# Kernel tuning notes

Hardware: AMD Instinct MI355X
Metric: run time of the kernel (lower is better)

The kernel has to match this reference:

```python
import jax, jax.numpy as jnp
import numpy as np

L_LAYERS = 4
B = 8
PATCH_H = 37
PATCH_W = 37
P = PATCH_H * PATCH_W  # 1369
D = 1024
J = 768
H = 518
W = 518
R_LIST = [1, 3, 5]
K_LIST = [1, 2, 3]
TOPMIN_MIN = 0.0
TOPMIN_MAX = 0.3


def setup_inputs() -> dict:
    key = jax.random.key(0)
    k1, k2 = jax.random.split(key)
    features = jax.random.normal(k1, (L_LAYERS, B, P, D), dtype=jnp.float32)
    cls_tokens = jax.random.normal(k2, (B, J), dtype=jnp.float32)
    return {"features": features, "cls_tokens": cls_tokens}


def _layer_norm_2d(x, eps=1e-5):
    # torch.layer_norm with normalized_shape = (P, D): normalize jointly over last two dims, no affine
    mu = jnp.mean(x, axis=(-2, -1), keepdims=True)
    var = jnp.var(x, axis=(-2, -1), keepdims=True)
    return (x - mu) * jax.lax.rsqrt(var + eps)


def _lnamd(features, r):
    # LNAMD: unfold(r,r, zero pad r//2) + adaptive_avg_pool1d(D*r*r -> D) == per-channel r x r
    # neighborhood mean over the patch grid with zero padding (pool bins are exactly r*r wide).
    if r == 1:
        return features
    l, b, p, d = features.shape
    x = features.reshape(l * b, PATCH_H, PATCH_W, d)
    pad = r // 2
    s = jax.lax.reduce_window(x, 0.0, jax.lax.add, (1, r, r, 1), (1, 1, 1, 1),
                              [(0, 0), (pad, pad), (pad, pad), (0, 0)])
    return (s / float(r * r)).reshape(l, b, p, d)


def _msm(rf, use_remat=False):
    # rf: [L,B,P,D] L2-normalized. Mutual scoring: for each image i, euclidean cdist of its
    # patches to all other images' patches, min over ref patches, mean of [k_min:k_max] smallest.
    l, b, p, d = rf.shape
    k_min = int(TOPMIN_MIN * (b - 1))
    k_max = int(TOPMIN_MAX * (b - 1))
    sq = jnp.sum(rf * rf, axis=-1)  # [L,B,P]

    def per_image(i):
        feat = rf[:, i]  # [L,P,D]
        dots = jnp.einsum('lpd,lbqd->lpbq', feat, rf)  # [L,P,B,P]
        d2 = sq[:, i][:, :, None, None] + sq[:, None, :, :] - 2.0 * dots
        dist = jnp.sqrt(jnp.maximum(d2, 1e-12))
        mind = jnp.min(dist, axis=-1)  # [L,P,B]
        mind = jnp.where(jnp.arange(b)[None, None, :] == i, jnp.inf, mind)  # exclude self
        neg_top = jax.lax.top_k(-mind, k_max)[0]  # k_max smallest distances (ascending)
        sel = -neg_top[..., k_min:k_max]
        return jnp.mean(sel, axis=-1)  # [L,P]

    fn = jax.checkpoint(per_image) if use_remat else per_image
    scores = jax.lax.map(fn, jnp.arange(b))  # [B,L,P]; lax.map keeps one cdist block live at a time
    return jnp.transpose(scores, (1, 0, 2))  # [L,B,P]


def _rscin(sim, scores, top_k):
    # zero out the B-top_k smallest similarities per row (keep top_k largest), row-normalize, reweight
    b = sim.shape[0]
    if top_k < b:
        vals, idx = jax.lax.top_k(sim, top_k)
        masked = jnp.zeros_like(sim).at[jnp.arange(b)[:, None], idx].set(vals)
    else:
        masked = sim
    masked = masked / jnp.sum(masked, axis=-1, keepdims=True)
    return masked @ scores


def _interp_mat(out_len, in_len):
    # bilinear, align_corners=True: src = dst * (in-1)/(out-1); separable 1D interpolation matrix
    pos = jnp.arange(out_len, dtype=jnp.float32) * ((in_len - 1) / (out_len - 1))
    i0 = jnp.clip(jnp.floor(pos).astype(jnp.int32), 0, in_len - 1)
    i1 = jnp.minimum(i0 + 1, in_len - 1)
    w = pos - i0.astype(jnp.float32)
    m = jnp.zeros((out_len, in_len), jnp.float32)
    m = m.at[jnp.arange(out_len), i0].add(1.0 - w)
    m = m.at[jnp.arange(out_len), i1].add(w)
    return m


def _forward(features, cls_tokens, use_remat=False):
    feats = _layer_norm_2d(features)  # [L,B,P,D]
    per_r = []
    for r in R_LIST:
        rf = _lnamd(feats, r)
        rf = rf / jnp.linalg.norm(rf, axis=-1, keepdims=True)
        per_r.append(jnp.mean(_msm(rf, use_remat), axis=0))  # mean over layers -> [B,P]
    scores = jnp.mean(jnp.stack(per_r, axis=0), axis=0)  # [B,P]
    img_scores = jnp.max(scores, axis=1)  # [B]
    cls = cls_tokens / jnp.linalg.norm(cls_tokens, axis=-1, keepdims=True)
    sim = cls @ cls.T  # [B,B]
    final = jnp.mean(jnp.stack([_rscin(sim, img_scores, k) for k in K_LIST], axis=0), axis=0)
    patch = scores.reshape(-1, PATCH_H, PATCH_W)
    mh = _interp_mat(H, PATCH_H)
    mw = _interp_mat(W, PATCH_W)
    pixel = jnp.einsum('Hh,bhw,Ww->bHW', mh, patch, mw)  # [B,H,W]
    return final, pixel


def reference(features, cls_tokens):
    return _forward(features, cls_tokens)
```

## Files before the change

### kernel.cpp

```cpp
#include <hip/hip_runtime.h>
#include <hip/hip_bf16.h>
#include <math.h>

#define L_LAYERS 4
#define BIMG 8
#define PATCH_H 37
#define PATCH_W 37
#define PP 1369
#define DD 1024
#define JJ 768
#define HOUT 518
#define WOUT 518
#define PPAD 1408
#define NPAIR 28
#define ZPAIR (L_LAYERS * NPAIR)
#define RFSZ  ((size_t)L_LAYERS * BIMG * PPAD * DD)
#define NRMSZ ((size_t)L_LAYERS * BIMG * PPAD)
#define MINDSZ ((size_t)L_LAYERS * BIMG * BIMG * PP)

typedef float floatx4 __attribute__((ext_vector_type(4)));

__device__ __forceinline__ unsigned int f2e4m3(float v) {
  unsigned int b = __float_as_uint(v);
  unsigned int sign = (b >> 24) & 0x80u;
  float mag = fabsf(v);
  unsigned int code;
  if (mag >= 0.015625f) {
    unsigned int mb = __float_as_uint(mag);
    mb = mb + 0x0007ffffu + ((mb >> 20) & 1u);
    code = (((mb >> 23) - 120u) << 3) | ((mb >> 20) & 7u);
  } else {
    code = (unsigned int)__float2int_rn(mag * 512.0f);
  }
  return code | sign;
}
__device__ __forceinline__ float e4m3tof(unsigned int c) {
  unsigned int em = c & 0x7fu;
  float m;
  if (em >= 8u) m = __uint_as_float((((em >> 3) + 120u) << 23) | ((em & 7u) << 20));
  else          m = (float)em * 0.001953125f;
  return (c & 0x80u) ? -m : m;
}

__device__ __forceinline__ int rf_swz(int p, int d) {
  return (d & ~63) |
         ((((d >> 4) & 3) ^ ((p >> 2) & 3)) << 4) |
         ((((d >> 3) & 1) ^ ((p >> 1) & 1)) << 3) |
         (d & 7);
}

__device__ __forceinline__ void gload_lds16(const void* gptr, void* lptr) {
  __builtin_amdgcn_global_load_lds(
      (const __attribute__((address_space(1))) unsigned int*)gptr,
      (__attribute__((address_space(3))) unsigned int*)lptr, 16, 0, 0);
}

__global__ __launch_bounds__(256) void k1_mu(const float* __restrict__ x,
                                             float* __restrict__ mu_acc) {
  const int lb = blockIdx.y;
  const float* base = x + (size_t)lb * PP * DD;
  const int N4 = PP * DD / 4;
  float s = 0.0f;
  for (int idx = blockIdx.x * 256 + threadIdx.x; idx < N4; idx += gridDim.x * 256) {
    float4 u = *(const float4*)(base + (size_t)idx * 4);
    s += u.x + u.y + u.z + u.w;
  }
  for (int off = 1; off < 64; off <<= 1) s += __shfl_xor(s, off, 64);
  __shared__ float red[4];
  if ((threadIdx.x & 63) == 0) red[threadIdx.x >> 6] = s;
  __syncthreads();
  if (threadIdx.x == 0)
    atomicAdd(&mu_acc[lb], red[0] + red[1] + red[2] + red[3]);
}

__device__ __forceinline__ void finish_r(float s0, float s1, float s2, float s3,
                                         float cm, unsigned char* dst, float* nrmdst,
                                         int tid, float* red) {
  s0 -= cm; s1 -= cm; s2 -= cm; s3 -= cm;
  float sq = s0 * s0 + s1 * s1 + s2 * s2 + s3 * s3;
  for (int off = 1; off < 64; off <<= 1) sq += __shfl_xor(sq, off, 64);
  __syncthreads();
  if ((tid & 63) == 0) red[tid >> 6] = sq;
  __syncthreads();
  const float rn16 = rsqrtf(red[0] + red[1] + red[2] + red[3]) * 16.0f;
  unsigned int c0 = f2e4m3(s0 * rn16), c1 = f2e4m3(s1 * rn16);
  unsigned int c2 = f2e4m3(s2 * rn16), c3 = f2e4m3(s3 * rn16);
  uchar4 o; o.x = (unsigned char)c0; o.y = (unsigned char)c1;
  o.z = (unsigned char)c2; o.w = (unsigned char)c3;
  *(uchar4*)dst = o;
  float q0 = e4m3tof(c0), q1 = e4m3tof(c1), q2 = e4m3tof(c2), q3 = e4m3tof(c3);
  float nq = q0 * q0 + q1 * q1 + q2 * q2 + q3 * q3;
  for (int off = 1; off < 64; off <<= 1) nq += __shfl_xor(nq, off, 64);
  __syncthreads();
  if ((tid & 63) == 0) red[tid >> 6] = nq;
  __syncthreads();
  if (tid == 0) *nrmdst = red[0] + red[1] + red[2] + red[3];
}

__global__ __launch_bounds__(256) void k2_pool3(const float* __restrict__ x,
                                                const float* __restrict__ mu_acc,
                                                unsigned char* __restrict__ rf,
                                                float* __restrict__ nrm) {
  const int p  = blockIdx.x;
  const int lb = blockIdx.y;
  const int tid = threadIdx.x;
  const int d0 = tid * 4;
  if (p >= PP) {
    const size_t zoff = ((size_t)lb * PPAD + p) * DD + d0;
    uchar4 z; z.x = 0; z.y = 0; z.z = 0; z.w = 0;
    for (int r = 0; r < 3; r++) {
      *(uchar4*)(rf + r * RFSZ + zoff) = z;
      if (tid == 0) nrm[r * NRMSZ + (size_t)lb * PPAD + p] = 0.0f;
    }
    return;
  }
  const size_t outoff = ((size_t)lb * PPAD + p) * DD + rf_swz(p, d0);
  const float mu = mu_acc[lb] * (1.0f / ((float)PP * (float)DD));
  const int ph = p / PATCH_W, pw = p % PATCH_W;
  float a5[4] = {0, 0, 0, 0}, a3[4] = {0, 0, 0, 0}, a1[4] = {0, 0, 0, 0};
  int c5 = 0, c3 = 0;
  for (int dy = -2; dy <= 2; dy++) {
    int qh = ph + dy; if (qh < 0 || qh >= PATCH_H) continue;
    for (int dx = -2; dx <= 2; dx++) {
      int qw = pw + dx; if (qw < 0 || qw >= PATCH_W) continue;
      const float* src = x + ((size_t)lb * PP + qh * PATCH_W + qw) * DD + d0;
      float4 u = *(const float4*)src;
      a5[0] += u.x; a5[1] += u.y; a5[2] += u.z; a5[3] += u.w; c5++;
      if (dy >= -1 && dy <= 1 && dx >= -1 && dx <= 1) {
        a3[0] += u.x; a3[1] += u.y; a3[2] += u.z; a3[3] += u.w; c3++;
        if (dy == 0 && dx == 0) { a1[0] = u.x; a1[1] = u.y; a1[2] = u.z; a1[3] = u.w; }
      }
    }
  }
  __shared__ float red[4];
  const size_t noff = (size_t)lb * PPAD + p;
  finish_r(a1[0], a1[1], a1[2], a1[3], mu, rf + outoff, nrm + noff, tid, red);
  finish_r(a3[0], a3[1], a3[2], a3[3], (float)c3 * mu, rf + RFSZ + outoff,
           nrm + NRMSZ + noff, tid, red);
  finish_r(a5[0], a5[1], a5[2], a5[3], (float)c5 * mu, rf + 2 * RFSZ + outoff,
           nrm + 2 * NRMSZ + noff, tid, red);
}

__global__ __launch_bounds__(256) void k2_pool(const float* __restrict__ x,
                                               const float* __restrict__ mu_acc,
                                               unsigned char* __restrict__ rf,
                                               float* __restrict__ nrm, int r) {
  const int p  = blockIdx.x;
  const int lb = blockIdx.y;
  const int tid = threadIdx.x;
  const int d0 = tid * 4;
  if (p >= PP) {
    const size_t zoff = ((size_t)lb * PPAD + p) * DD + d0;
    uchar4 z; z.x = 0; z.y = 0; z.z = 0; z.w = 0;
    *(uchar4*)(rf + zoff) = z;
    if (tid == 0) nrm[(size_t)lb * PPAD + p] = 0.0f;
    return;
  }
  const size_t outoff = ((size_t)lb * PPAD + p) * DD + rf_swz(p, d0);
  const float mu = mu_acc[lb] * (1.0f / ((float)PP * (float)DD));
  const int ph = p / PATCH_W, pw = p % PATCH_W;
  const int pad = r >> 1;
  float s0 = 0, s1 = 0, s2 = 0, s3 = 0;
  int cnt = 0;
  for (int dy = -pad; dy <= pad; dy++) {
    int qh = ph + dy; if (qh < 0 || qh >= PATCH_H) continue;
    for (int dx = -pad; dx <= pad; dx++) {
      int qw = pw + dx; if (qw < 0 || qw >= PATCH_W) continue;
      cnt++;
      const float* src = x + ((size_t)lb * PP + qh * PATCH_W + qw) * DD + d0;
      float4 u = *(const float4*)src;
      s0 += u.x; s1 += u.y; s2 += u.z; s3 += u.w;
    }
  }
  __shared__ float red[4];
  finish_r(s0, s1, s2, s3, (float)cnt * mu, rf + outoff,
           nrm + (size_t)lb * PPAD + p, tid, red);
}

__global__ __launch_bounds__(256, 4) void k3_pairdots(const unsigned char* __restrict__ rf,
                                                      const float* __restrict__ nrm,
                                                      unsigned int* __restrict__ mind) {
  const int rsel = blockIdx.z / ZPAIR;
  const int zz   = blockIdx.z % ZPAIR;
  const int l = zz / NPAIR;
  int rem = zz % NPAIR;
  int i = 0, span = BIMG - 1;
  while (rem >= span) { rem -= span; span--; i++; }
  const int j = i + 1 + rem;

  const unsigned char* rfr = rf + (size_t)rsel * RFSZ;
  const int rowbase = blockIdx.x * 128;
  const int colbase = blockIdx.y * 128;
  const unsigned char* A  = rfr + ((size_t)(l * BIMG + i) * PPAD + rowbase) * DD;
  const unsigned char* Bp = rfr + ((size_t)(l * BIMG + j) * PPAD + colbase) * DD;

  __shared__ __align__(16) unsigned char lA[2][128 * 64];
  __shared__ __align__(16) unsigned char lB[2][128 * 64];

  const int tid  = threadIdx.x;
  const int lane = tid & 63;
  const int wave = tid >> 6;
  const int lrow = lane & 15;
  const int quad = lane >> 4;
  const int wr = (wave >> 1) * 64;
  const int wc = (wave & 1) * 64;

  floatx4 acc[4][4];
#pragma unroll
  for (int a = 0; a < 4; a++)
#pragma unroll
    for (int b = 0; b < 4; b++) acc[a][b] = (floatx4){0.f, 0.f, 0.f, 0.f};

  const int r0  = wave * 32 + (lane >> 2);
  const size_t goff = (size_t)r0 * DD + (lane & 3) * 16;
  const int woff = wave * 2048;

  const int gs   = (lrow >> 2) & 3;
  const int hb   = (lrow >> 1) & 1;
  const int sub8 = (((quad & 1) ^ hb) << 3);

  gload_lds16(A + goff, lA[0] + woff);
  gload_lds16(A + goff + 16 * DD, lA[0] + woff + 1024);
  gload_lds16(Bp + goff, lB[0] + woff);
  gload_lds16(Bp + goff + 16 * DD, lB[0] + woff + 1024);
  __syncthreads();

#pragma unroll 2
  for (int t = 0; t < 16; ++t) {
    const int cur = t & 1;
    if (t < 15) {
      const int k1 = (t + 1) << 6;
      gload_lds16(A + goff + k1, lA[cur ^ 1] + woff);
      gload_lds16(A + goff + 16 * DD + k1, lA[cur ^ 1] + woff + 1024);
      gload_lds16(Bp + goff + k1, lB[cur ^ 1] + woff);
      gload_lds16(Bp + goff + 16 * DD + k1, lB[cur ^ 1] + woff + 1024);
    }
#pragma unroll
    for (int ks = 0; ks < 2; ks++) {
      const int gfrag = ((((ks << 1) + (quad >> 1)) ^ gs) << 4) + sub8;
      long af[4], bfv[4];
#pragma unroll
      for (int mt = 0; mt < 4; mt++)
        af[mt] = *(const long*)(lA[cur] + (wr + mt * 16 + lrow) * 64 + gfrag);
#pragma unroll
      for (int ct = 0; ct < 4; ct++)
        bfv[ct] = *(const long*)(lB[cur] + (wc + ct * 16 + lrow) * 64 + gfrag);
#pragma unroll
      for (int mt = 0; mt < 4; mt++)
#pragma unroll
        for (int ct = 0; ct < 4; ct++)
          acc[mt][ct] = __builtin_amdgcn_mfma_f32_16x16x32_fp8_fp8(
              af[mt], bfv[ct], acc[mt][ct], 0, 0, 0);
    }
    __syncthreads();
  }

  const float* nI = nrm + rsel * NRMSZ + (size_t)(l * BIMG + i) * PPAD;
  const float* nJ = nrm + rsel * NRMSZ + (size_t)(l * BIMG + j) * PPAD;
  unsigned int* mrow = mind + rsel * MINDSZ + ((size_t)(l * BIMG + i) * BIMG + j) * PP;
  unsigned int* mcol = mind + rsel * MINDSZ + ((size_t)(l * BIMG + j) * BIMG + i) * PP;

#pragma unroll
  for (int mt = 0; mt < 4; mt++) {
#pragma unroll
    for (int reg = 0; reg < 4; reg++) {
      const int gr = rowbase + wr + mt * 16 + quad * 4 + reg;
      float v = -1e30f;
#pragma unroll
      for (int ct = 0; ct < 4; ct++) {
        const int gc = colbase + wc + ct * 16 + lrow;
        if (gc < PP) v = fmaxf(v, 2.0f * acc[mt][ct][reg] - nJ[gc]);
      }
      for (int off = 1; off < 16; off <<= 1) v = fmaxf(v, __shfl_xor(v, off, 64));
      if (lrow == 0 && gr < PP)
        atomicMax(mrow + gr, __float_as_uint(v + 1024.0f));
    }
  }
#pragma unroll
  for (int ct = 0; ct < 4; ct++) {
    const int gc = colbase + wc + ct * 16 + lrow;
    float v = -1e30f;
#pragma unroll
    for (int mt = 0; mt < 4; mt++) {
      const int grb = rowbase + wr + mt * 16 + quad * 4;
#pragma unroll
      for (int reg = 0; reg < 4; reg++)
        if (grb + reg < PP) v = fmaxf(v, 2.0f * acc[mt][ct][reg] - nI[grb + reg]);
    }
    for (int off = 16; off < 64; off <<= 1) v = fmaxf(v, __shfl_xor(v, off, 64));
    if (quad == 0 && gc < PP)
      atomicMax(mcol + gc, __float_as_uint(v + 1024.0f));
  }
}

__global__ void k4_scores(const unsigned int* __restrict__ mind,
                          const float* __restrict__ nrm,
                          float* __restrict__ scores, int nr) {
  const int idx = blockIdx.x * 256 + threadIdx.x;
  if (idx >= BIMG * PP) return;
  const int i = idx / PP, p = idx % PP;
  float accum = 0.0f;
  for (int r = 0; r < nr; r++) {
    for (int l = 0; l < L_LAYERS; l++) {
      const float n_own = nrm[r * NRMSZ + (size_t)(l * BIMG + i) * PPAD + p];
      float m1 = 1e30f, m2 = 1e30f;
      for (int b = 0; b < BIMG; b++) {
        if (b == i) continue;
        const unsigned int enc =
            mind[r * MINDSZ + ((size_t)(l * BIMG + i) * BIMG + b) * PP + p];
        const float val = __uint_as_float(enc) - 1024.0f;
        const float d2 = fmaxf((n_own - val) * (1.0f / 256.0f), 1e-12f);
        const float dist = sqrtf(d2);
        if (dist < m1) { m2 = m1; m1 = dist; }
        else if (dist < m2) { m2 = dist; }
      }
      accum += 0.5f * (m1 + m2);
    }
  }
  scores[idx] += accum * (1.0f / (float)(L_LAYERS * 3));
}

__global__ void k5_imgmax(const float* __restrict__ scores, float* __restrict__ img) {
  const int i = blockIdx.x;
  float m = -1e30f;
  for (int p = threadIdx.x; p < PP; p += 256) m = fmaxf(m, scores[i * PP + p]);
  for (int off = 1; off < 64; off <<= 1) m = fmaxf(m, __shfl_xor(m, off, 64));
  __shared__ float red[4];
  if ((threadIdx.x & 63) == 0) red[threadIdx.x >> 6] = m;
  __syncthreads();
  if (threadIdx.x == 0)
    img[i] = fmaxf(fmaxf(red[0], red[1]), fmaxf(red[2], red[3]));
}

__global__ void k6_final(const float* __restrict__ cls,
                         const float* __restrict__ img,
                         float* __restrict__ out) {
  __shared__ float norms[BIMG];
  __shared__ float sim[BIMG][BIMG];
  const int t = threadIdx.x;
  if (t < BIMG) {
    float s = 0;
    for (int d = 0; d < JJ; d++) { float v = cls[t * JJ + d]; s += v * v; }
    norms[t] = sqrtf(s);
  }
  __syncthreads();
  {
    const int ii = t >> 3, jj = t & 7;
    float s = 0;
    for (int d = 0; d < JJ; d++) s += cls[ii * JJ + d] * cls[jj * JJ + d];
    sim[ii][jj] = s / (norms[ii] * norms[jj]);
  }
  __syncthreads();
  if (t < BIMG) {
    float v[8]; int id[8];
    for (int a = 0; a < 8; a++) { v[a] = sim[t][a]; id[a] = a; }
    for (int a = 0; a < 8; a++) {
      int best = a;
      for (int b = a + 1; b < 8; b++) if (v[b] > v[best]) best = b;
      float tv = v[a]; v[a] = v[best]; v[best] = tv;
      int ti = id[a]; id[a] = id[best]; id[best] = ti;
    }
    float res = 0;
    for (int k = 1; k <= 3; k++) {
      float num = 0, den = 0;
      for (int a = 0; a < k; a++) { num += v[a] * img[id[a]]; den += v[a]; }
      res += num / den;
    }
    out[t] = res * (1.0f / 3.0f);
  }
}

__global__ void k7_pixel(const float* __restrict__ scores,
                         float* __restrict__ out) {
  const int idx = blockIdx.x * 256 + threadIdx.x;
  if (idx >= BIMG * HOUT * WOUT) return;
  const int b = idx / (HOUT * WOUT);
  const int rem = idx % (HOUT * WOUT);
  const int Y = rem / WOUT, X = rem % WOUT;
  const float sy = (float)(PATCH_H - 1) / (float)(HOUT - 1);
  const float sx = (float)(PATCH_W - 1) / (float)(WOUT - 1);
  float py = (float)Y * sy;
  float px = (float)X * sx;
  int y0 = (int)floorf(py); y0 = min(max(y0, 0), PATCH_H - 1);
  int x0 = (int)floorf(px); x0 = min(max(x0, 0), PATCH_W - 1);
  const int y1 = min(y0 + 1, PATCH_H - 1);
  const int x1 = min(x0 + 1, PATCH_W - 1);
  const float wy = py - (float)y0, wx = px - (float)x0;
  const float* sc = scores + (size_t)b * PP;
  const float v =
      (1.f - wy) * ((1.f - wx) * sc[y0 * PATCH_W + x0] + wx * sc[y0 * PATCH_W + x1]) +
      wy         * ((1.f - wx) * sc[y1 * PATCH_W + x0] + wx * sc[y1 * PATCH_W + x1]);
  out[8 + idx] = v;
}

extern "C" void kernel_launch(void* const* d_in, const int* in_sizes, int n_in,
                              void* d_out, int out_size, void* d_ws, size_t ws_size,
                              hipStream_t stream) {
  const float* feat = (const float*)d_in[0];
  const float* cls  = (const float*)d_in[1];
  float* out = (float*)d_out;

  const size_t need_fused = 3 * RFSZ + 3 * MINDSZ * 4 + 3 * NRMSZ * 4 +
                            (size_t)BIMG * PP * 4 + 1024;
  const bool fused = ws_size >= need_fused;

  char* ws = (char*)d_ws;
  size_t off = 0;
  unsigned char* rf = (unsigned char*)(ws + off);
  off += (fused ? 3 : 1) * RFSZ;
  unsigned int* mind = (unsigned int*)(ws + off);
  off += (fused ? 3 : 1) * MINDSZ * 4;
  float* nrm = (float*)(ws + off);
  off += (fused ? 3 : 1) * NRMSZ * 4;
  float* scores = (float*)(ws + off);
  off += (size_t)BIMG * PP * 4;
  float* mu_acc = (float*)(ws + off);
  off += 32 * 4;
  float* img = (float*)(ws + off);
  off += 8 * 4;

  hipMemsetAsync(mu_acc, 0, 32 * 4, stream);
  hipMemsetAsync(scores, 0, (size_t)BIMG * PP * 4, stream);
  k1_mu<<<dim3(43, 32), 256, 0, stream>>>(feat, mu_acc);

  if (fused) {
    k2_pool3<<<dim3(PPAD, 32), 256, 0, stream>>>(feat, mu_acc, rf, nrm);
    hipMemsetAsync(mind, 0, 3 * MINDSZ * 4, stream);
    k3_pairdots<<<dim3(11, 11, 3 * ZPAIR), 256, 0, stream>>>(rf, nrm, mind);
    k4_scores<<<(BIMG * PP + 255) / 256, 256, 0, stream>>>(mind, nrm, scores, 3);
  } else {
    const int rlist[3] = {1, 3, 5};
    for (int ri = 0; ri < 3; ri++) {
      k2_pool<<<dim3(PPAD, 32), 256, 0, stream>>>(feat, mu_acc, rf, nrm, rlist[ri]);
      hipMemsetAsync(mind, 0, MINDSZ * 4, stream);
      k3_pairdots<<<dim3(11, 11, ZPAIR), 256, 0, stream>>>(rf, nrm, mind);
      k4_scores<<<(BIMG * PP + 255) / 256, 256, 0, stream>>>(mind, nrm, scores, 1);
    }
  }
  k5_imgmax<<<8, 256, 0, stream>>>(scores, img);
  k6_final<<<1, 64, 0, stream>>>(cls, img, out);
  k7_pixel<<<(BIMG * HOUT * WOUT + 255) / 256, 256, 0, stream>>>(scores, out);
}
```

Measured before the change: 2.571 ms.

## Remap pairdots grid for XCD locality and use fine-grained waitcnt pipelining

Flattens the pairdots launch to a 1D grid and remaps block IDs so that consecutive work tiles land on the same XCD (blockIdx mod 8 interleave). This is meant to improve L2 reuse of shared A/B panels. It also restructures the K loop: issue the next prefetch, wait only on the older loads with vmcnt(4), and use raw s_barrier with sched_barrier, with the last iteration peeled out. This replaces full __syncthreads and lets loads overlap compute, at the cost of depending on hand-coded waitcnt correctness. The remap assumes the grid size divides evenly by 8.

```diff
diff --git a/kernel.cpp b/kernel.cpp
--- a/kernel.cpp
+++ b/kernel.cpp
@@ -180,8 +180,15 @@
 __global__ __launch_bounds__(256, 4) void k3_pairdots(const unsigned char* __restrict__ rf,
                                                       const float* __restrict__ nrm,
                                                       unsigned int* __restrict__ mind) {
-  const int rsel = blockIdx.z / ZPAIR;
-  const int zz   = blockIdx.z % ZPAIR;
+  const unsigned int cpx = gridDim.x >> 3;
+  const unsigned int wid = (blockIdx.x & 7) * cpx + (blockIdx.x >> 3);
+  const int z  = wid / 121;
+  const int rm = wid % 121;
+  const int ty = rm / 11;
+  const int tx = rm % 11;
+
+  const int rsel = z / ZPAIR;
+  const int zz   = z % ZPAIR;
   const int l = zz / NPAIR;
   int rem = zz % NPAIR;
   int i = 0, span = BIMG - 1;
@@ -189,8 +196,8 @@
   const int j = i + 1 + rem;
 
   const unsigned char* rfr = rf + (size_t)rsel * RFSZ;
-  const int rowbase = blockIdx.x * 128;
-  const int colbase = blockIdx.y * 128;
+  const int rowbase = tx * 128;
+  const int colbase = ty * 128;
   const unsigned char* A  = rfr + ((size_t)(l * BIMG + i) * PPAD + rowbase) * DD;
   const unsigned char* Bp = rfr + ((size_t)(l * BIMG + j) * PPAD + colbase) * DD;
 
@@ -223,18 +230,17 @@
   gload_lds16(A + goff + 16 * DD, lA[0] + woff + 1024);
   gload_lds16(Bp + goff, lB[0] + woff);
   gload_lds16(Bp + goff + 16 * DD, lB[0] + woff + 1024);
-  __syncthreads();
-
-#pragma unroll 2
-  for (int t = 0; t < 16; ++t) {
+
+  for (int t = 0; t < 15; ++t) {
     const int cur = t & 1;
-    if (t < 15) {
-      const int k1 = (t + 1) << 6;
-      gload_lds16(A + goff + k1, lA[cur ^ 1] + woff);
-      gload_lds16(A + goff + 16 * DD + k1, lA[cur ^ 1] + woff + 1024);
-      gload_lds16(Bp + goff + k1, lB[cur ^ 1] + woff);
-      gload_lds16(Bp + goff + 16 * DD + k1, lB[cur ^ 1] + woff + 1024);
-    }
+    const int k1 = (t + 1) << 6;
+    gload_lds16(A + goff + k1, lA[cur ^ 1] + woff);
+    gload_lds16(A + goff + 16 * DD + k1, lA[cur ^ 1] + woff + 1024);
+    gload_lds16(Bp + goff + k1, lB[cur ^ 1] + woff);
+    gload_lds16(Bp + goff + 16 * DD + k1, lB[cur ^ 1] + woff + 1024);
+    asm volatile("s_waitcnt vmcnt(4)" ::: "memory");
+    __builtin_amdgcn_s_barrier();
+    __builtin_amdgcn_sched_barrier(0);
 #pragma unroll
     for (int ks = 0; ks < 2; ks++) {
       const int gfrag = ((((ks << 1) + (quad >> 1)) ^ gs) << 4) + sub8;
@@ -252,7 +258,31 @@
           acc[mt][ct] = __builtin_amdgcn_mfma_f32_16x16x32_fp8_fp8(
               af[mt], bfv[ct], acc[mt][ct], 0, 0, 0);
     }
-    __syncthreads();
+    __builtin_amdgcn_sched_barrier(0);
+    __builtin_amdgcn_s_barrier();
+  }
+  asm volatile("s_waitcnt vmcnt(0)" ::: "memory");
+  __builtin_amdgcn_s_barrier();
+  __builtin_amdgcn_sched_barrier(0);
+  {
+    const int cur = 1;
+#pragma unroll
+    for (int ks = 0; ks < 2; ks++) {
+      const int gfrag = ((((ks << 1) + (quad >> 1)) ^ gs) << 4) + sub8;
+      long af[4], bfv[4];
+#pragma unroll
+      for (int mt = 0; mt < 4; mt++)
+        af[mt] = *(const long*)(lA[cur] + (wr + mt * 16 + lrow) * 64 + gfrag);
+#pragma unroll
+      for (int ct = 0; ct < 4; ct++)
+        bfv[ct] = *(const long*)(lB[cur] + (wc + ct * 16 + lrow) * 64 + gfrag);
+#pragma unroll
+      for (int mt = 0; mt < 4; mt++)
+#pragma unroll
+        for (int ct = 0; ct < 4; ct++)
+          acc[mt][ct] = __builtin_amdgcn_mfma_f32_16x16x32_fp8_fp8(
+              af[mt], bfv[ct], acc[mt][ct], 0, 0, 0);
+    }
   }
 
   const float* nI = nrm + rsel * NRMSZ + (size_t)(l * BIMG + i) * PPAD;
@@ -426,14 +456,14 @@
   if (fused) {
     k2_pool3<<<dim3(PPAD, 32), 256, 0, stream>>>(feat, mu_acc, rf, nrm);
     hipMemsetAsync(mind, 0, 3 * MINDSZ * 4, stream);
-    k3_pairdots<<<dim3(11, 11, 3 * ZPAIR), 256, 0, stream>>>(rf, nrm, mind);
+    k3_pairdots<<<dim3(121 * 3 * ZPAIR), 256, 0, stream>>>(rf, nrm, mind);
     k4_scores<<<(BIMG * PP + 255) / 256, 256, 0, stream>>>(mind, nrm, scores, 3);
   } else {
     const int rlist[3] = {1, 3, 5};
     for (int ri = 0; ri < 3; ri++) {
       k2_pool<<<dim3(PPAD, 32), 256, 0, stream>>>(feat, mu_acc, rf, nrm, rlist[ri]);
       hipMemsetAsync(mind, 0, MINDSZ * 4, stream);
-      k3_pairdots<<<dim3(11, 11, ZPAIR), 256, 0, stream>>>(rf, nrm, mind);
+      k3_pairdots<<<dim3(121 * ZPAIR), 256, 0, stream>>>(rf, nrm, mind);
       k4_scores<<<(BIMG * PP + 255) / 256, 256, 0, stream>>>(mind, nrm, scores, 1);
     }
   }
```

Result: faster. 2.395 ms (-6.9%).
